# Kernel tuning notes

Measured on AMD Instinct MI355X. Metric: run time of the kernel, lower is better.

Reference implementation:

```python
import jax, jax.numpy as jnp
import numpy as np

DIM = 128
NUM_HEADS = 8
HEAD_DIM = DIM // NUM_HEADS
SCALE = HEAD_DIM ** -0.5


def _attn_branch(xs, Wq, bq, Wp, bp):
    # xs: (N, L, C) batch of sequences; Q=K=V=q (per the module)
    N, L, C = xs.shape
    q = xs @ Wq + bq                                   # (N, L, C)
    q = q.reshape(N, L, NUM_HEADS, HEAD_DIM).transpose(0, 2, 1, 3)  # (N, h, L, d)
    qs = q * SCALE
    attn = jax.nn.softmax(jnp.einsum('nhld,nhmd->nhlm', qs, qs), axis=-1)
    out = jnp.einsum('nhlm,nhmd->nhld', attn, q)       # (N, h, L, d)
    out = out.transpose(0, 2, 1, 3).reshape(N, L, C)
    return out @ Wp + bp


def setup_inputs() -> dict:
    key = jax.random.key(0)
    ks = jax.random.split(key, 12)
    B, C, D, H, W = 1, DIM, 31, 32, 32
    s = 0.02
    return {
        'x': jax.random.normal(ks[0], (B, C, D, H, W), jnp.float32),
        'Wq_spec': jax.random.normal(ks[1], (C, C), jnp.float32) * s,
        'bq_spec': jnp.zeros((C,), jnp.float32),
        'Wp_spec': jax.random.normal(ks[2], (C, C), jnp.float32) * s,
        'bp_spec': jnp.zeros((C,), jnp.float32),
        'Wq_spat': jax.random.normal(ks[3], (C, C), jnp.float32) * s,
        'bq_spat': jnp.zeros((C,), jnp.float32),
        'Wp_spat': jax.random.normal(ks[4], (C, C), jnp.float32) * s,
        'bp_spat': jnp.zeros((C,), jnp.float32),
        'Wg': jax.random.normal(ks[5], (2 * C, C), jnp.float32) * s,
        'bg': jnp.zeros((C,), jnp.float32),
    }


def reference(x, Wq_spec, bq_spec, Wp_spec, bp_spec,
              Wq_spat, bq_spat, Wp_spat, bp_spat, Wg, bg):
    B, C, D, H, W = x.shape
    # ---- spectral branch: sequences of length D per spatial position ----
    x_spec = x.transpose(0, 3, 4, 2, 1).reshape(B * H * W, D, C)
    out_spec = _attn_branch(x_spec, Wq_spec, bq_spec, Wp_spec, bp_spec)
    out_spectral = out_spec.reshape(B, H, W, D, C).transpose(0, 4, 3, 1, 2)  # (B,C,D,H,W)
    # ---- spatial branch: sequences of length H*W per band ----
    x_spat = x.transpose(0, 2, 3, 4, 1).reshape(B * D, H * W, C)
    out_spat = _attn_branch(x_spat, Wq_spat, bq_spat, Wp_spat, bp_spat)
    out_spatial = out_spat.reshape(B, D, H, W, C).transpose(0, 4, 1, 2, 3)   # (B,C,D,H,W)
    # ---- sigmoid-gated fusion (global average pooled gate) ----
    gi = jnp.concatenate([
        out_spectral.mean(axis=(2, 3, 4)),
        out_spatial.mean(axis=(2, 3, 4)),
    ], axis=-1)                                          # (B, 2C)
    gate = jax.nn.sigmoid(gi @ Wg + bg)[:, :, None, None, None]  # (B,C,1,1,1)
    return gate * out_spectral + (1.0 - gate) * out_spatial
```

## Files before the change

### kernel.cpp

```cpp
#include <hip/hip_runtime.h>
#include <cstddef>

#define CC 128
#define NH 8
#define HD 16
#define DDIM 31
#define HWW 1024
#define TOK 31744
#define SCALE2 0.0625f

typedef __attribute__((ext_vector_type(4))) short  short4v;
typedef __attribute__((ext_vector_type(4))) float  float4v;

__device__ inline unsigned bf16rne(float f) {
    unsigned u = __float_as_uint(f);
    return (u + 0x7fffu + ((u >> 16) & 1u)) >> 16;
}
__device__ inline float bf2f(unsigned h) { return __uint_as_float(h << 16); }

__device__ inline unsigned packsplit(float v) {
    unsigned h = bf16rne(v);
    unsigned l = bf16rne(v - bf2f(h));
    return h | (l << 16);
}
__device__ inline uint2 pack_hi4(uint4 p) {
    return make_uint2((p.x & 0xffffu) | (p.y << 16),
                      (p.z & 0xffffu) | (p.w << 16));
}
__device__ inline uint2 pack_lo4(uint4 p) {
    return make_uint2((p.x >> 16) | (p.y & 0xffff0000u),
                      (p.z >> 16) | (p.w & 0xffff0000u));
}

__device__ inline void load_wfrags(const float* __restrict__ W, int co0, int l,
                                   int quad, short4v* ah, short4v* al)
{
#pragma unroll
    for (int k8 = 0; k8 < 8; ++k8) {
#pragma unroll
        for (int j = 0; j < 4; ++j) {
            float w = W[(size_t)(k8 * 16 + quad * 4 + j) * CC + co0 + l];
            unsigned h = bf16rne(w);
            ah[k8][j] = (short)h;
            al[k8][j] = (short)bf16rne(w - bf2f(h));
        }
    }
}

#define AST 132

__global__ __launch_bounds__(512, 2) void qproj_kernel(
    const float* __restrict__ x,
    const float* __restrict__ Wq1, const float* __restrict__ Wq2,
    const float* __restrict__ bq1, const float* __restrict__ bq2,
    unsigned* __restrict__ q1p, unsigned* __restrict__ q2p,
    float* __restrict__ sums)
{
    __shared__ ushort sbuf[2 * CC * AST];
    ushort* Ahi = sbuf;
    ushort* Alo = sbuf + CC * AST;
    unsigned* S = (unsigned*)sbuf;
    const int tid = threadIdx.x;
    const int t0  = blockIdx.x * 128;
    if (blockIdx.x == 0 && tid < 2 * CC) sums[tid] = 0.f;

    for (int i = tid; i < CC * 128 / 4; i += 512) {
        int t4 = i & 31, ci = i >> 5;
        float4 v = *(const float4*)&x[(size_t)ci * TOK + t0 + t4 * 4];
        float xv[4] = {v.x, v.y, v.z, v.w};
#pragma unroll
        for (int e = 0; e < 4; ++e) {
            unsigned h = bf16rne(xv[e]);
            unsigned lw = bf16rne(xv[e] - bf2f(h));
            Ahi[(t4 * 4 + e) * AST + ci] = (ushort)h;
            Alo[(t4 * 4 + e) * AST + ci] = (ushort)lw;
        }
    }
    __syncthreads();

    const int lane = tid & 63;
    const int l    = lane & 15;
    const int quad = lane >> 4;
    const int co0  = (tid >> 6) * 16;

    short4v ah[2][8], al[2][8];
    load_wfrags(Wq1, co0, l, quad, ah[0], al[0]);
    load_wfrags(Wq2, co0, l, quad, ah[1], al[1]);
    float4v acc[2][8];
#pragma unroll
    for (int br = 0; br < 2; ++br)
#pragma unroll
        for (int nt = 0; nt < 8; ++nt) acc[br][nt] = (float4v){0.f, 0.f, 0.f, 0.f};
#pragma unroll
    for (int k8 = 0; k8 < 8; ++k8) {
#pragma unroll
        for (int nt = 0; nt < 8; ++nt) {
            short4v bh = *(const short4v*)&Ahi[(nt * 16 + l) * AST + k8 * 16 + quad * 4];
            short4v bl = *(const short4v*)&Alo[(nt * 16 + l) * AST + k8 * 16 + quad * 4];
            acc[0][nt] = __builtin_amdgcn_mfma_f32_16x16x16bf16_1k(ah[0][k8], bh, acc[0][nt], 0, 0, 0);
            acc[0][nt] = __builtin_amdgcn_mfma_f32_16x16x16bf16_1k(ah[0][k8], bl, acc[0][nt], 0, 0, 0);
            acc[0][nt] = __builtin_amdgcn_mfma_f32_16x16x16bf16_1k(al[0][k8], bh, acc[0][nt], 0, 0, 0);
            acc[1][nt] = __builtin_amdgcn_mfma_f32_16x16x16bf16_1k(ah[1][k8], bh, acc[1][nt], 0, 0, 0);
            acc[1][nt] = __builtin_amdgcn_mfma_f32_16x16x16bf16_1k(ah[1][k8], bl, acc[1][nt], 0, 0, 0);
            acc[1][nt] = __builtin_amdgcn_mfma_f32_16x16x16bf16_1k(al[1][k8], bh, acc[1][nt], 0, 0, 0);
        }
    }

    for (int branch = 0; branch < 2; ++branch) {
        const float* bq = branch ? bq2 : bq1;
        unsigned* op    = branch ? q2p : q1p;
        float4 bv = *(const float4*)&bq[co0 + quad * 4];
        float bb[4] = {bv.x, bv.y, bv.z, bv.w};
        __syncthreads();
#pragma unroll
        for (int nt = 0; nt < 8; ++nt) {
#pragma unroll
            for (int reg = 0; reg < 4; ++reg)
                S[(nt * 16 + l) * AST + co0 + quad * 4 + reg] =
                    packsplit(acc[branch][nt][reg] + bb[reg]);
        }
        __syncthreads();
        for (int i = tid; i < 128 * 32; i += 512) {
            int t = i >> 5, c4 = i & 31;
            uint4 pv = *(const uint4*)&S[t * AST + c4 * 4];
            *(uint4*)&op[(size_t)(t0 + t) * CC + c4 * 4] = pv;
        }
    }
}

#define QS2 132
#define QSS 20
#define QTP 1044
__global__ __launch_bounds__(1024, 4) void attn_kernel(
    unsigned* __restrict__ q1p, unsigned* __restrict__ q2p,
    float* __restrict__ sums)
{
    __shared__ __align__(16) ushort smem[HWW * QSS + HD * QTP];
    __shared__ float fsum[CC];
    const int tid  = threadIdx.x;
    const int lane = tid & 63;
    const int l    = lane & 15;
    const int quad = lane >> 4;
    const float k2 = SCALE2 * 1.44269504f;
    const short4v onesb = {(short)0x3F80, (short)0x3F80, (short)0x3F80, (short)0x3F80};
    if (tid < CC) fsum[tid] = 0.f;

    {
        const int d = blockIdx.x >> 3, h = blockIdx.x & 7;
        ushort* Qs  = smem;
        ushort* QTs = smem + HWW * QSS;
        const size_t base = (size_t)d * HWW * CC + h * HD;

        for (int i = tid; i < HWW * 4; i += 1024) {
            int row = i >> 2, q4 = i & 3;
            uint4 p = *(const uint4*)&q2p[base + (size_t)row * CC + q4 * 4];
            *(uint2*)&Qs[row * QSS + q4 * 4] = pack_hi4(p);
            QTs[(q4 * 4 + 0) * QTP + row] = (ushort)p.x;
            QTs[(q4 * 4 + 1) * QTP + row] = (ushort)p.y;
            QTs[(q4 * 4 + 2) * QTP + row] = (ushort)p.z;
            QTs[(q4 * 4 + 3) * QTP + row] = (ushort)p.w;
        }
        __syncthreads();

        const int Rw = (tid >> 6) * 64;
        short4v qf[4];
#pragma unroll
        for (int lt = 0; lt < 4; ++lt) {
            short4v raw = *(short4v*)&Qs[(Rw + lt * 16 + l) * QSS + quad * 4];
            short4v sc;
#pragma unroll
            for (int e = 0; e < 4; ++e) {
                float f = bf2f((unsigned)(ushort)raw[e]) * k2;
                sc[e] = (short)bf16rne(f);
            }
            qf[lt] = sc;
        }

        float4v acc[4], accs[4];
#pragma unroll
        for (int lt = 0; lt < 4; ++lt) {
            acc[lt]  = (float4v){0.f, 0.f, 0.f, 0.f};
            accs[lt] = (float4v){0.f, 0.f, 0.f, 0.f};
        }

#pragma unroll 2
        for (int mt = 0; mt < 64; ++mt) {
            const int m0 = mt * 16;
            short4v ka = *(short4v*)&Qs[(m0 + l) * QSS + quad * 4];
            short4v vb = *(short4v*)&QTs[l * QTP + m0 + quad * 4];
#pragma unroll
            for (int lt = 0; lt < 4; ++lt) {
                float4v s = __builtin_amdgcn_mfma_f32_16x16x16bf16_1k(
                    ka, qf[lt], (float4v){0.f, 0.f, 0.f, 0.f}, 0, 0, 0);
                unsigned u0 = __float_as_uint(__builtin_amdgcn_exp2f(s[0]));
                unsigned u1 = __float_as_uint(__builtin_amdgcn_exp2f(s[1]));
                unsigned u2 = __float_as_uint(__builtin_amdgcn_exp2f(s[2]));
                unsigned u3 = __float_as_uint(__builtin_amdgcn_exp2f(s[3]));
                short4v pf;
                pf[0] = (short)(u0 >> 16); pf[1] = (short)(u1 >> 16);
                pf[2] = (short)(u2 >> 16); pf[3] = (short)(u3 >> 16);
                acc[lt]  = __builtin_amdgcn_mfma_f32_16x16x16bf16_1k(vb, pf, acc[lt], 0, 0, 0);
                accs[lt] = __builtin_amdgcn_mfma_f32_16x16x16bf16_1k(onesb, pf, accs[lt], 0, 0, 0);
            }
        }

        float vsum[4] = {0.f, 0.f, 0.f, 0.f};
#pragma unroll
        for (int lt = 0; lt < 4; ++lt) {
            float inv = 1.f / accs[lt][0];
            int token = Rw + lt * 16 + l;
            float v0 = acc[lt][0] * inv, v1 = acc[lt][1] * inv;
            float v2 = acc[lt][2] * inv, v3 = acc[lt][3] * inv;
            uint4 pv;
            pv.x = packsplit(v0); pv.y = packsplit(v1);
            pv.z = packsplit(v2); pv.w = packsplit(v3);
            *(uint4*)&q2p[base + (size_t)token * CC + quad * 4] = pv;
            vsum[0] += v0; vsum[1] += v1; vsum[2] += v2; vsum[3] += v3;
        }
#pragma unroll
        for (int reg = 0; reg < 4; ++reg) {
            float v = vsum[reg];
            v += __shfl_xor(v, 1); v += __shfl_xor(v, 2);
            v += __shfl_xor(v, 4); v += __shfl_xor(v, 8);
            if (l == 0) atomicAdd(&fsum[quad * 4 + reg], v);
        }
        __syncthreads();
        if (tid < HD) atomicAdd(&sums[CC + h * HD + tid], fsum[tid]);
    }

    const int half_id = blockIdx.x >> 1;
    const bool has_job = (blockIdx.x & 1) ? (half_id < 4) : (half_id < 124);
    if (!has_job) return;
    const int job = (blockIdx.x & 1) ? (124 + half_id) : half_id;
    const int hw0 = job * 8;

    __syncthreads();
    if (tid < CC) fsum[tid] = 0.f;

    const int wave = tid >> 6;
    const int hwl  = wave >> 1;
    const int half = wave & 1;
    const int hw   = hw0 + hwl;
    ushort* Q = smem + hwl * (32 * QS2);
    for (int it = 0; it < 8; ++it) {
        int idx = it * 64 + lane;
        int dd = half * 16 + (idx >> 5), c4 = idx & 31;
        if (dd < 31) {
            uint4 p = *(const uint4*)&q1p[((size_t)dd * HWW + hw) * CC + c4 * 4];
            *(uint2*)&Q[dd * QS2 + c4 * 4] = pack_hi4(p);
        }
    }
    if (half) for (int i = lane; i < 128; i += 64) Q[31 * QS2 + i] = 0;
    __syncthreads();

    const int hh = half * 4;
#pragma unroll
    for (int hl = 0; hl < 4; ++hl) {
        const int hc = (hh + hl) * HD;
        short4v qf[2];
        qf[0] = *(const short4v*)&Q[l * QS2 + hc + quad * 4];
        qf[1] = *(const short4v*)&Q[(16 + l) * QS2 + hc + quad * 4];
        short4v va[2];
#pragma unroll
        for (int j = 0; j < 2; ++j)
#pragma unroll
            for (int jj = 0; jj < 4; ++jj)
                va[j][jj] = (short)Q[(j * 16 + quad * 4 + jj) * QS2 + hc + l];

        float4v o[2]   = {(float4v){0.f,0.f,0.f,0.f}, (float4v){0.f,0.f,0.f,0.f}};
        float4v osr[2] = {(float4v){0.f,0.f,0.f,0.f}, (float4v){0.f,0.f,0.f,0.f}};
#pragma unroll
        for (int j = 0; j < 2; ++j) {
#pragma unroll
            for (int i2 = 0; i2 < 2; ++i2) {
                float4v s = __builtin_amdgcn_mfma_f32_16x16x16bf16_1k(
                    qf[j], qf[i2], (float4v){0.f,0.f,0.f,0.f}, 0, 0, 0);
                unsigned u0 = __float_as_uint(__builtin_amdgcn_exp2f(s[0] * k2));
                unsigned u1 = __float_as_uint(__builtin_amdgcn_exp2f(s[1] * k2));
                unsigned u2 = __float_as_uint(__builtin_amdgcn_exp2f(s[2] * k2));
                unsigned u3 = __float_as_uint(__builtin_amdgcn_exp2f(s[3] * k2));
                if (j == 1 && quad == 3) u3 = 0;
                short4v pf;
                pf[0] = (short)(u0 >> 16); pf[1] = (short)(u1 >> 16);
                pf[2] = (short)(u2 >> 16); pf[3] = (short)(u3 >> 16);
                o[i2]   = __builtin_amdgcn_mfma_f32_16x16x16bf16_1k(va[j], pf, o[i2], 0, 0, 0);
                osr[i2] = __builtin_amdgcn_mfma_f32_16x16x16bf16_1k(onesb, pf, osr[i2], 0, 0, 0);
            }
        }
        float vsum[4] = {0.f, 0.f, 0.f, 0.f};
#pragma unroll
        for (int i2 = 0; i2 < 2; ++i2) {
            float inv = 1.f / osr[i2][0];
            int dq = i2 * 16 + l;
            if (dq < 31) {
                uint4 pv;
                float v0 = o[i2][0] * inv, v1 = o[i2][1] * inv;
                float v2 = o[i2][2] * inv, v3 = o[i2][3] * inv;
                pv.x = packsplit(v0); pv.y = packsplit(v1);
                pv.z = packsplit(v2); pv.w = packsplit(v3);
                *(uint4*)&q1p[((size_t)dq * HWW + hw) * CC + hc + quad * 4] = pv;
                vsum[0] += v0; vsum[1] += v1; vsum[2] += v2; vsum[3] += v3;
            }
        }
#pragma unroll
        for (int r = 0; r < 4; ++r) {
            float v = vsum[r];
            v += __shfl_xor(v, 1); v += __shfl_xor(v, 2);
            v += __shfl_xor(v, 4); v += __shfl_xor(v, 8);
            if (l == 0) atomicAdd(&fsum[hc + quad * 4 + r], v);
        }
    }
    __syncthreads();
    if (tid < CC) atomicAdd(&sums[tid], fsum[tid]);
}

__global__ __launch_bounds__(512, 2) void oproj_kernel(
    const unsigned* __restrict__ q1p, const unsigned* __restrict__ q2p,
    const float* __restrict__ Wp1, const float* __restrict__ Wp2,
    const float* __restrict__ bp1, const float* __restrict__ bp2,
    const float* __restrict__ Wg,  const float* __restrict__ bg,
    const float* __restrict__ sums, float* __restrict__ out)
{
    __shared__ ushort sbuf[2 * 64 * AST];
    ushort* Ahi = sbuf;
    ushort* Alo = sbuf + 64 * AST;
    unsigned* S = (unsigned*)sbuf;
    __shared__ float pa[4][CC];
    __shared__ float giv[2 * CC];
    __shared__ float gf[CC];
    const int tid = threadIdx.x;
    const int t0  = blockIdx.x * 64;
    const int lane = tid & 63;
    const int l    = lane & 15;
    const int quad = lane >> 4;
    const int co0  = (tid >> 6) * 16;

    {
        const int part = tid >> 7, c = tid & 127;
        const float* Wp = (part < 2) ? Wp1 : Wp2;
        const float* sp = (part < 2) ? sums : sums + CC;
        const int k0 = (part & 1) * 64;
        float a = 0.f;
        for (int kk = 0; kk < 64; ++kk) {
            int k = k0 + kk;
            a += sp[k] * Wp[(size_t)k * CC + c];
        }
        pa[part][c] = a;
        __syncthreads();
        if (tid < 2 * CC) {
            float m = (tid < CC) ? (pa[0][tid] + pa[1][tid])
                                 : (pa[2][tid - CC] + pa[3][tid - CC]);
            float bb = (tid < CC) ? bp1[tid] : bp2[tid - CC];
            giv[tid] = m * (1.f / (float)TOK) + bb;
        }
        __syncthreads();
        float b = 0.f;
        for (int kk = 0; kk < 64; ++kk) {
            int j = part * 64 + kk;
            b += giv[j] * Wg[(size_t)j * CC + c];
        }
        pa[part][c] = b;
        __syncthreads();
        if (tid < CC)
            gf[tid] = 1.f / (1.f + __expf(-(bg[tid] + pa[0][tid] + pa[1][tid] +
                                           pa[2][tid] + pa[3][tid])));
    }

    float4v acc[2][4];
#pragma unroll
    for (int br = 0; br < 2; ++br)
#pragma unroll
        for (int nt = 0; nt < 4; ++nt) acc[br][nt] = (float4v){0.f, 0.f, 0.f, 0.f};

    for (int br = 0; br < 2; ++br) {
        const unsigned* Ap = br ? q2p : q1p;
        const float*    W  = br ? Wp2 : Wp1;
        short4v ah[8], al[8];
        load_wfrags(W, co0, l, quad, ah, al);
        __syncthreads();
        for (int i = tid; i < 64 * 32; i += 512) {
            int t = i >> 5, c4 = i & 31;
            uint4 p = *(const uint4*)&Ap[(size_t)(t0 + t) * CC + c4 * 4];
            *(uint2*)&Ahi[t * AST + c4 * 4] = pack_hi4(p);
            *(uint2*)&Alo[t * AST + c4 * 4] = pack_lo4(p);
        }
        __syncthreads();
#pragma unroll
        for (int k8 = 0; k8 < 8; ++k8) {
#pragma unroll
            for (int nt = 0; nt < 4; ++nt) {
                short4v bh = *(const short4v*)&Ahi[(nt * 16 + l) * AST + k8 * 16 + quad * 4];
                short4v bl = *(const short4v*)&Alo[(nt * 16 + l) * AST + k8 * 16 + quad * 4];
                acc[br][nt] = __builtin_amdgcn_mfma_f32_16x16x16bf16_1k(ah[k8], bh, acc[br][nt], 0, 0, 0);
                acc[br][nt] = __builtin_amdgcn_mfma_f32_16x16x16bf16_1k(ah[k8], bl, acc[br][nt], 0, 0, 0);
                acc[br][nt] = __builtin_amdgcn_mfma_f32_16x16x16bf16_1k(al[k8], bh, acc[br][nt], 0, 0, 0);
            }
        }
    }

    float4 b1 = *(const float4*)&bp1[co0 + quad * 4];
    float4 b2 = *(const float4*)&bp2[co0 + quad * 4];
    float bb1[4] = {b1.x, b1.y, b1.z, b1.w};
    float bb2[4] = {b2.x, b2.y, b2.z, b2.w};
    float gg[4];
#pragma unroll
    for (int e = 0; e < 4; ++e) gg[e] = gf[co0 + quad * 4 + e];

    __syncthreads();
#pragma unroll
    for (int nt = 0; nt < 4; ++nt) {
        int tl = nt * 16 + l;
#pragma unroll
        for (int reg = 0; reg < 4; ++reg) {
            float v = gg[reg] * (acc[0][nt][reg] + bb1[reg]) +
                      (1.f - gg[reg]) * (acc[1][nt][reg] + bb2[reg]);
            S[(co0 + quad * 4 + reg) * 66 + tl] = __float_as_uint(v);
        }
    }
    __syncthreads();
    for (int i = tid; i < 128 * 32; i += 512) {
        int co = i >> 5, t2 = i & 31;
        uint2 v = *(const uint2*)&S[co * 66 + t2 * 2];
        *(uint2*)&out[(size_t)co * TOK + t0 + t2 * 2] = v;
    }
}

extern "C" void kernel_launch(void* const* d_in, const int* in_sizes, int n_in,
                              void* d_out, int out_size, void* d_ws, size_t ws_size,
                              hipStream_t stream)
{
    const float* x   = (const float*)d_in[0];
    const float* Wq1 = (const float*)d_in[1];
    const float* bq1 = (const float*)d_in[2];
    const float* Wp1 = (const float*)d_in[3];
    const float* bp1 = (const float*)d_in[4];
    const float* Wq2 = (const float*)d_in[5];
    const float* bq2 = (const float*)d_in[6];
    const float* Wp2 = (const float*)d_in[7];
    const float* bp2 = (const float*)d_in[8];
    const float* Wg  = (const float*)d_in[9];
    const float* bg  = (const float*)d_in[10];
    float* out = (float*)d_out;

    unsigned* q1p = (unsigned*)d_ws;
    unsigned* q2p = q1p + (size_t)TOK * CC;
    float*   sums = (float*)(q2p + (size_t)TOK * CC);

    qproj_kernel<<<dim3(248), 512, 0, stream>>>(x, Wq1, Wq2, bq1, bq2,
                                                q1p, q2p, sums);
    attn_kernel<<<dim3(248), 1024, 0, stream>>>(q1p, q2p, sums);
    oproj_kernel<<<dim3(496), 512, 0, stream>>>(q1p, q2p,
                                                Wp1, Wp2, bp1, bp2, Wg, bg,
                                                sums, out);
}
```

Measured before the change: 177.1 us.

## Split spatial attention query rows across two blocks and halve qproj token tile

The spatial attention kernel gets a SPLIT template mode where each (band, head) pair is handled by two blocks, each taking half the query rows. The result goes to a separate output buffer so the other half can still read the unmodified Q, and the kernel launches 496 blocks instead of 248. The qproj kernel now tiles 64 tokens per block, doubling its grid, and both qproj and oproj raise their launch-bounds occupancy hint. The P-fragment packing uses v_perm instead of shifts. The split path depends on a larger workspace, and each block still redundantly loads the full 1024-row Q tile into shared memory.

```diff
diff --git a/kernel.cpp b/kernel.cpp
--- a/kernel.cpp
+++ b/kernel.cpp
@@ -8,9 +8,11 @@
 #define HWW 1024
 #define TOK 31744
 #define SCALE2 0.0625f
+#define QTOK 64
 
 typedef __attribute__((ext_vector_type(4))) short  short4v;
 typedef __attribute__((ext_vector_type(4))) float  float4v;
+typedef __attribute__((ext_vector_type(2))) unsigned uint2v;
 
 __device__ inline unsigned bf16rne(float f) {
     unsigned u = __float_as_uint(f);
@@ -30,6 +32,14 @@
 __device__ inline uint2 pack_lo4(uint4 p) {
     return make_uint2((p.x >> 16) | (p.y & 0xffff0000u),
                       (p.z >> 16) | (p.w & 0xffff0000u));
+}
+
+__device__ inline short4v pack_pf(unsigned u0, unsigned u1,
+                                  unsigned u2, unsigned u3) {
+    uint2v pd;
+    pd[0] = __builtin_amdgcn_perm(u1, u0, 0x07060302u);
+    pd[1] = __builtin_amdgcn_perm(u3, u2, 0x07060302u);
+    return __builtin_bit_cast(short4v, pd);
 }
 
 __device__ inline void load_wfrags(const float* __restrict__ W, int co0, int l,
@@ -49,23 +59,23 @@
 
 #define AST 132
 
-__global__ __launch_bounds__(512, 2) void qproj_kernel(
+__global__ __launch_bounds__(512, 4) void qproj_kernel(
     const float* __restrict__ x,
     const float* __restrict__ Wq1, const float* __restrict__ Wq2,
     const float* __restrict__ bq1, const float* __restrict__ bq2,
     unsigned* __restrict__ q1p, unsigned* __restrict__ q2p,
     float* __restrict__ sums)
 {
-    __shared__ ushort sbuf[2 * CC * AST];
+    __shared__ ushort sbuf[2 * QTOK * AST];
     ushort* Ahi = sbuf;
-    ushort* Alo = sbuf + CC * AST;
+    ushort* Alo = sbuf + QTOK * AST;
     unsigned* S = (unsigned*)sbuf;
     const int tid = threadIdx.x;
-    const int t0  = blockIdx.x * 128;
+    const int t0  = blockIdx.x * QTOK;
     if (blockIdx.x == 0 && tid < 2 * CC) sums[tid] = 0.f;
 
-    for (int i = tid; i < CC * 128 / 4; i += 512) {
-        int t4 = i & 31, ci = i >> 5;
+    for (int i = tid; i < CC * QTOK / 4; i += 512) {
+        int t4 = i & 15, ci = i >> 4;
         float4 v = *(const float4*)&x[(size_t)ci * TOK + t0 + t4 * 4];
         float xv[4] = {v.x, v.y, v.z, v.w};
 #pragma unroll
@@ -86,15 +96,15 @@
     short4v ah[2][8], al[2][8];
     load_wfrags(Wq1, co0, l, quad, ah[0], al[0]);
     load_wfrags(Wq2, co0, l, quad, ah[1], al[1]);
-    float4v acc[2][8];
+    float4v acc[2][4];
 #pragma unroll
     for (int br = 0; br < 2; ++br)
 #pragma unroll
-        for (int nt = 0; nt < 8; ++nt) acc[br][nt] = (float4v){0.f, 0.f, 0.f, 0.f};
+        for (int nt = 0; nt < 4; ++nt) acc[br][nt] = (float4v){0.f, 0.f, 0.f, 0.f};
 #pragma unroll
     for (int k8 = 0; k8 < 8; ++k8) {
 #pragma unroll
-        for (int nt = 0; nt < 8; ++nt) {
+        for (int nt = 0; nt < 4; ++nt) {
             short4v bh = *(const short4v*)&Ahi[(nt * 16 + l) * AST + k8 * 16 + quad * 4];
             short4v bl = *(const short4v*)&Alo[(nt * 16 + l) * AST + k8 * 16 + quad * 4];
             acc[0][nt] = __builtin_amdgcn_mfma_f32_16x16x16bf16_1k(ah[0][k8], bh, acc[0][nt], 0, 0, 0);
@@ -113,14 +123,14 @@
         float bb[4] = {bv.x, bv.y, bv.z, bv.w};
         __syncthreads();
 #pragma unroll
-        for (int nt = 0; nt < 8; ++nt) {
+        for (int nt = 0; nt < 4; ++nt) {
 #pragma unroll
             for (int reg = 0; reg < 4; ++reg)
                 S[(nt * 16 + l) * AST + co0 + quad * 4 + reg] =
                     packsplit(acc[branch][nt][reg] + bb[reg]);
         }
         __syncthreads();
-        for (int i = tid; i < 128 * 32; i += 512) {
+        for (int i = tid; i < QTOK * 32; i += 512) {
             int t = i >> 5, c4 = i & 31;
             uint4 pv = *(const uint4*)&S[t * AST + c4 * 4];
             *(uint4*)&op[(size_t)(t0 + t) * CC + c4 * 4] = pv;
@@ -131,10 +141,12 @@
 #define QS2 132
 #define QSS 20
 #define QTP 1044
-__global__ __launch_bounds__(1024, 4) void attn_kernel(
-    unsigned* __restrict__ q1p, unsigned* __restrict__ q2p,
-    float* __restrict__ sums)
+template<int SPLIT>
+__global__ __launch_bounds__(1024, SPLIT ? 8 : 4) void attn_kernel(
+    unsigned* __restrict__ q1p, const unsigned* q2p,
+    unsigned* q2out, float* __restrict__ sums)
 {
+    constexpr int NLT = SPLIT ? 2 : 4;
     __shared__ __align__(16) ushort smem[HWW * QSS + HD * QTP];
     __shared__ float fsum[CC];
     const int tid  = threadIdx.x;
@@ -146,7 +158,9 @@
     if (tid < CC) fsum[tid] = 0.f;
 
     {
-        const int d = blockIdx.x >> 3, h = blockIdx.x & 7;
+        const int sp    = SPLIT ? (int)(blockIdx.x >> 1) : (int)blockIdx.x;
+        const int qhalf = SPLIT ? (int)(blockIdx.x & 1) : 0;
+        const int d = sp >> 3, h = sp & 7;
         ushort* Qs  = smem;
         ushort* QTs = smem + HWW * QSS;
         const size_t base = (size_t)d * HWW * CC + h * HD;
@@ -162,10 +176,10 @@
         }
         __syncthreads();
 
-        const int Rw = (tid >> 6) * 64;
-        short4v qf[4];
-#pragma unroll
-        for (int lt = 0; lt < 4; ++lt) {
+        const int Rw = qhalf * 512 + (tid >> 6) * (NLT * 16);
+        short4v qf[NLT];
+#pragma unroll
+        for (int lt = 0; lt < NLT; ++lt) {
             short4v raw = *(short4v*)&Qs[(Rw + lt * 16 + l) * QSS + quad * 4];
             short4v sc;
 #pragma unroll
@@ -176,9 +190,9 @@
             qf[lt] = sc;
         }
 
-        float4v acc[4], accs[4];
-#pragma unroll
-        for (int lt = 0; lt < 4; ++lt) {
+        float4v acc[NLT], accs[NLT];
+#pragma unroll
+        for (int lt = 0; lt < NLT; ++lt) {
             acc[lt]  = (float4v){0.f, 0.f, 0.f, 0.f};
             accs[lt] = (float4v){0.f, 0.f, 0.f, 0.f};
         }
@@ -189,16 +203,14 @@
             short4v ka = *(short4v*)&Qs[(m0 + l) * QSS + quad * 4];
             short4v vb = *(short4v*)&QTs[l * QTP + m0 + quad * 4];
 #pragma unroll
-            for (int lt = 0; lt < 4; ++lt) {
+            for (int lt = 0; lt < NLT; ++lt) {
                 float4v s = __builtin_amdgcn_mfma_f32_16x16x16bf16_1k(
                     ka, qf[lt], (float4v){0.f, 0.f, 0.f, 0.f}, 0, 0, 0);
                 unsigned u0 = __float_as_uint(__builtin_amdgcn_exp2f(s[0]));
                 unsigned u1 = __float_as_uint(__builtin_amdgcn_exp2f(s[1]));
                 unsigned u2 = __float_as_uint(__builtin_amdgcn_exp2f(s[2]));
                 unsigned u3 = __float_as_uint(__builtin_amdgcn_exp2f(s[3]));
-                short4v pf;
-                pf[0] = (short)(u0 >> 16); pf[1] = (short)(u1 >> 16);
-                pf[2] = (short)(u2 >> 16); pf[3] = (short)(u3 >> 16);
+                short4v pf = pack_pf(u0, u1, u2, u3);
                 acc[lt]  = __builtin_amdgcn_mfma_f32_16x16x16bf16_1k(vb, pf, acc[lt], 0, 0, 0);
                 accs[lt] = __builtin_amdgcn_mfma_f32_16x16x16bf16_1k(onesb, pf, accs[lt], 0, 0, 0);
             }
@@ -206,7 +218,7 @@
 
         float vsum[4] = {0.f, 0.f, 0.f, 0.f};
 #pragma unroll
-        for (int lt = 0; lt < 4; ++lt) {
+        for (int lt = 0; lt < NLT; ++lt) {
             float inv = 1.f / accs[lt][0];
             int token = Rw + lt * 16 + l;
             float v0 = acc[lt][0] * inv, v1 = acc[lt][1] * inv;
@@ -214,7 +226,7 @@
             uint4 pv;
             pv.x = packsplit(v0); pv.y = packsplit(v1);
             pv.z = packsplit(v2); pv.w = packsplit(v3);
-            *(uint4*)&q2p[base + (size_t)token * CC + quad * 4] = pv;
+            *(uint4*)&q2out[base + (size_t)token * CC + quad * 4] = pv;
             vsum[0] += v0; vsum[1] += v1; vsum[2] += v2; vsum[3] += v3;
         }
 #pragma unroll
@@ -228,10 +240,19 @@
         if (tid < HD) atomicAdd(&sums[CC + h * HD + tid], fsum[tid]);
     }
 
-    const int half_id = blockIdx.x >> 1;
-    const bool has_job = (blockIdx.x & 1) ? (half_id < 4) : (half_id < 124);
+    int job;
+    bool has_job;
+    if (SPLIT) {
+        const int m4  = blockIdx.x & 3;
+        const int q4b = blockIdx.x >> 2;
+        has_job = (m4 == 0) ? (q4b < 124) : ((m4 == 2) && (q4b < 4));
+        job = (m4 == 0) ? q4b : (124 + q4b);
+    } else {
+        const int half_id = blockIdx.x >> 1;
+        has_job = (blockIdx.x & 1) ? (half_id < 4) : (half_id < 124);
+        job = (blockIdx.x & 1) ? (124 + half_id) : half_id;
+    }
     if (!has_job) return;
-    const int job = (blockIdx.x & 1) ? (124 + half_id) : half_id;
     const int hw0 = job * 8;
 
     __syncthreads();
@@ -280,9 +301,7 @@
                 unsigned u2 = __float_as_uint(__builtin_amdgcn_exp2f(s[2] * k2));
                 unsigned u3 = __float_as_uint(__builtin_amdgcn_exp2f(s[3] * k2));
                 if (j == 1 && quad == 3) u3 = 0;
-                short4v pf;
-                pf[0] = (short)(u0 >> 16); pf[1] = (short)(u1 >> 16);
-                pf[2] = (short)(u2 >> 16); pf[3] = (short)(u3 >> 16);
+                short4v pf = pack_pf(u0, u1, u2, u3);
                 o[i2]   = __builtin_amdgcn_mfma_f32_16x16x16bf16_1k(va[j], pf, o[i2], 0, 0, 0);
                 osr[i2] = __builtin_amdgcn_mfma_f32_16x16x16bf16_1k(onesb, pf, osr[i2], 0, 0, 0);
             }
@@ -314,7 +333,7 @@
     if (tid < CC) atomicAdd(&sums[tid], fsum[tid]);
 }
 
-__global__ __launch_bounds__(512, 2) void oproj_kernel(
+__global__ __launch_bounds__(512, 4) void oproj_kernel(
     const unsigned* __restrict__ q1p, const unsigned* __restrict__ q2p,
     const float* __restrict__ Wp1, const float* __restrict__ Wp2,
     const float* __restrict__ bp1, const float* __restrict__ bp2,
@@ -442,14 +461,20 @@
     const float* bg  = (const float*)d_in[10];
     float* out = (float*)d_out;
 
+    const size_t plane = (size_t)TOK * CC;
     unsigned* q1p = (unsigned*)d_ws;
-    unsigned* q2p = q1p + (size_t)TOK * CC;
-    float*   sums = (float*)(q2p + (size_t)TOK * CC);
-
-    qproj_kernel<<<dim3(248), 512, 0, stream>>>(x, Wq1, Wq2, bq1, bq2,
-                                                q1p, q2p, sums);
-    attn_kernel<<<dim3(248), 1024, 0, stream>>>(q1p, q2p, sums);
-    oproj_kernel<<<dim3(496), 512, 0, stream>>>(q1p, q2p,
+    unsigned* q2p = q1p + plane;
+    const bool split = ws_size >= (3 * plane * sizeof(unsigned) + 1024 * sizeof(float));
+    unsigned* q2pb = split ? (q2p + plane) : q2p;
+    float*   sums  = (float*)(q2pb + plane);
+
+    qproj_kernel<<<dim3(TOK / QTOK), 512, 0, stream>>>(x, Wq1, Wq2, bq1, bq2,
+                                                       q1p, q2p, sums);
+    if (split)
+        attn_kernel<1><<<dim3(496), 1024, 0, stream>>>(q1p, q2p, q2pb, sums);
+    else
+        attn_kernel<0><<<dim3(248), 1024, 0, stream>>>(q1p, q2p, q2p, sums);
+    oproj_kernel<<<dim3(496), 512, 0, stream>>>(q1p, q2pb,
                                                 Wp1, Wp2, bp1, bp2, Wg, bg,
                                                 sums, out);
 }
```

Result: slower. 181.3 us (+2.4%).
